# Performance work log

Hardware: AMD Instinct MI355X
Metric: run time of the kernel (lower is better)

Reference implementation:

```python
import jax, jax.numpy as jnp
import numpy as np

N = 100000   # nodes
E = 1600000  # edges
F = 256      # feature_dim
H = 64       # hidden_dim == out_channels
HEADS = 1


def setup_inputs() -> dict:
    key = jax.random.key(0)
    ks = jax.random.split(key, 12)
    x = jax.random.normal(ks[0], (N, F), dtype=jnp.float32)
    edge_index = jax.random.randint(ks[1], (2, E), 0, N, dtype=jnp.int32)
    s = 0.05
    params = {
        'W_proj': jax.random.normal(ks[2], (F, H), dtype=jnp.float32) * s,
        'b_proj': jnp.zeros((H,), dtype=jnp.float32),
        'Wq1': jax.random.normal(ks[3], (H, HEADS * H), dtype=jnp.float32) * s,
        'Wk1': jax.random.normal(ks[4], (H, HEADS * H), dtype=jnp.float32) * s,
        'Wv1': jax.random.normal(ks[5], (H, HEADS * H), dtype=jnp.float32) * s,
        'Wq2': jax.random.normal(ks[6], (H, HEADS * H), dtype=jnp.float32) * s,
        'Wk2': jax.random.normal(ks[7], (H, HEADS * H), dtype=jnp.float32) * s,
        'Wv2': jax.random.normal(ks[8], (H, HEADS * H), dtype=jnp.float32) * s,
        'W_sig': jax.random.normal(ks[9], (H, 1), dtype=jnp.float32) * s,
        'b_sig': jnp.zeros((1,), dtype=jnp.float32),
    }
    return {'x': x, 'edge_index': edge_index, **params}


def _gat_layer(x, src, dst, Wq, Wk, Wv):
    # x: [N, H]; src/dst: [E] (edge_index[0]=source j, edge_index[1]=dest i)
    n = x.shape[0]
    q = (x @ Wq).reshape(n, HEADS, H)
    k = (x @ Wk).reshape(n, HEADS, H)
    v = (x @ Wv).reshape(n, HEADS, H)
    # edge-wise scores: (q_i * k_j).sum(-1) / sqrt(out_channels)
    scores = jnp.einsum('ehc,ehc->eh', q[dst], k[src]) / np.float32(np.sqrt(H))
    alpha = jax.nn.relu(scores)                                  # [E, HEADS]
    # segment softmax over destination neighborhoods (numerically stable)
    m = jax.ops.segment_max(alpha, dst, num_segments=n)          # [N, HEADS]
    m = jnp.where(jnp.isfinite(m), m, jnp.float32(0.0))
    e = jnp.exp(alpha - m[dst])
    denom = jax.ops.segment_sum(e, dst, num_segments=n)
    a = e / (denom[dst] + jnp.float32(1e-16))                    # [E, HEADS]
    # scatter-weighted sum of values to destinations
    out = jax.ops.segment_sum(v[src] * a[:, :, None], dst, num_segments=n)
    return out.mean(axis=1), a                                   # [N, H], [E, HEADS]


def reference(x, edge_index, W_proj, b_proj, Wq1, Wk1, Wv1, Wq2, Wk2, Wv2, W_sig, b_sig):
    src, dst = edge_index[0], edge_index[1]
    h = jax.nn.gelu(x @ W_proj + b_proj, approximate=False)
    h, attn1 = _gat_layer(h, src, dst, Wq1, Wk1, Wv1)
    h = jax.nn.gelu(h, approximate=False)
    h, attn2 = _gat_layer(h, src, dst, Wq2, Wk2, Wv2)
    signals = h @ W_sig + b_sig                                  # [N, 1]
    return signals, attn1, attn2
```

## Files before the change

kernel.cpp:

```cpp
#include <hip/hip_runtime.h>
#include <hip/hip_fp16.h>
#include <math.h>

#define FF 256
#define HH 64

typedef __attribute__((ext_vector_type(8))) short short8;
typedef __attribute__((ext_vector_type(4))) float f32x4;

__device__ __forceinline__ float gelu_f(float x) {
    float ax = fabsf(x) * 0.70710678118654752f;
    float t = __builtin_amdgcn_rcpf(fmaf(0.3275911f, ax, 1.0f));
    float poly = t * fmaf(t, fmaf(t, fmaf(t, fmaf(t, 1.061405429f, -1.453152027f),
                  1.421413741f), -0.284496736f), 0.254829592f);
    float er = 1.0f - poly * __expf(-ax * ax);
    er = (x < 0.f) ? -er : er;
    return 0.5f * x * (1.0f + er);
}

__device__ __forceinline__ unsigned short bf16rne(float f) {
    unsigned u = __float_as_uint(f);
    unsigned r = u + 0x7FFFu + ((u >> 16) & 1u);
    return (unsigned short)(r >> 16);
}

__device__ __forceinline__ void bf16split(float f, short& hi, short& lo) {
    unsigned u = __float_as_uint(f);
    unsigned r = u + 0x7FFFu + ((u >> 16) & 1u);
    hi = (short)(r >> 16);
    float fh = __uint_as_float(r & 0xFFFF0000u);
    float fl = f - fh;
    unsigned u2 = __float_as_uint(fl);
    unsigned r2 = u2 + 0x7FFFu + ((u2 >> 16) & 1u);
    lo = (short)(r2 >> 16);
}

__device__ __forceinline__ __half2 shfl_xor_h2(__half2 v, int off) {
    union { __half2 h; int i; } u;
    u.h = v;
    u.i = __shfl_xor(u.i, off, 64);
    return u.h;
}

__global__ __launch_bounds__(256) void k_wprep(
        const float* __restrict__ Wp,
        const float* __restrict__ Wq1, const float* __restrict__ Wk1, const float* __restrict__ Wv1,
        const float* __restrict__ Wq2, const float* __restrict__ Wk2, const float* __restrict__ Wv2,
        short* __restrict__ wf) {
    int total = 16384 + 6 * 4096;
    for (int gid = blockIdx.x * 256 + threadIdx.x; gid < total; gid += gridDim.x * 256) {
        const float* W;
        int fid, hibase, lobase;
        if (gid < 16384) {
            W = Wp; fid = gid; hibase = 0; lobase = 16384;
        } else {
            int t = gid - 16384;
            int m = t >> 12;
            fid = t & 4095;
            switch (m) {
                case 0: W = Wq1; break;
                case 1: W = Wk1; break;
                case 2: W = Wv1; break;
                case 3: W = Wq2; break;
                case 4: W = Wk2; break;
                default: W = Wv2; break;
            }
            hibase = 32768 + m * 8192;
            lobase = hibase + 4096;
        }
        int j    = fid & 7;
        int lane = (fid >> 3) & 63;
        int ct   = (fid >> 9) & 3;
        int s    = fid >> 11;
        int k    = s * 32 + (lane >> 4) * 8 + j;
        int col  = ct * 16 + (lane & 15);
        short hi, lo;
        bf16split(W[k * HH + col], hi, lo);
        wf[hibase + fid] = hi;
        wf[lobase + fid] = lo;
    }
}

__device__ __forceinline__ void do_degree(int bid, const int* __restrict__ dst,
        int* __restrict__ deg, int* __restrict__ rank, int E) {
    int base = bid * 4096;
    if (base >= E) return;
    int e0 = base + threadIdx.x * 4;
    if (base + 4095 < E) {
        int4 d[4];
        #pragma unroll
        for (int i = 0; i < 4; ++i)
            d[i] = *reinterpret_cast<const int4*>(dst + e0 + i * 1024);
        int4 r[4];
        #pragma unroll
        for (int i = 0; i < 4; ++i) {
            r[i].x = atomicAdd(&deg[d[i].x], 1);
            r[i].y = atomicAdd(&deg[d[i].y], 1);
            r[i].z = atomicAdd(&deg[d[i].z], 1);
            r[i].w = atomicAdd(&deg[d[i].w], 1);
        }
        #pragma unroll
        for (int i = 0; i < 4; ++i)
            *reinterpret_cast<int4*>(rank + e0 + i * 1024) = r[i];
    } else {
        #pragma unroll
        for (int i = 0; i < 4; ++i)
            for (int j = 0; j < 4; ++j) {
                int e = e0 + i * 1024 + j;
                if (e < E) rank[e] = atomicAdd(&deg[dst[e]], 1);
            }
    }
}

__device__ __forceinline__ void do_fill(int bid, const int* __restrict__ src,
        const int* __restrict__ dst, const int* __restrict__ rowptr,
        const int* __restrict__ rank,
        int* __restrict__ esrc, int* __restrict__ inv, int E) {
    int base = bid * 4096;
    if (base >= E) return;
    int e0 = base + threadIdx.x * 4;
    if (base + 4095 < E) {
        int4 d[4], s[4], r[4];
        #pragma unroll
        for (int i = 0; i < 4; ++i) {
            d[i] = *reinterpret_cast<const int4*>(dst + e0 + i * 1024);
            s[i] = *reinterpret_cast<const int4*>(src + e0 + i * 1024);
            r[i] = *reinterpret_cast<const int4*>(rank + e0 + i * 1024);
        }
        int4 p[4];
        #pragma unroll
        for (int i = 0; i < 4; ++i) {
            p[i].x = rowptr[d[i].x] + r[i].x;
            p[i].y = rowptr[d[i].y] + r[i].y;
            p[i].z = rowptr[d[i].z] + r[i].z;
            p[i].w = rowptr[d[i].w] + r[i].w;
        }
        #pragma unroll
        for (int i = 0; i < 4; ++i) {
            esrc[p[i].x] = s[i].x;
            esrc[p[i].y] = s[i].y;
            esrc[p[i].z] = s[i].z;
            esrc[p[i].w] = s[i].w;
            *reinterpret_cast<int4*>(inv + e0 + i * 1024) = p[i];
        }
    } else {
        #pragma unroll
        for (int i = 0; i < 4; ++i)
            for (int j = 0; j < 4; ++j) {
                int e = e0 + i * 1024 + j;
                if (e < E) {
                    int pos = rowptr[dst[e]] + rank[e];
                    esrc[pos] = src[e];
                    inv[e] = pos;
                }
            }
    }
}

__device__ __forceinline__ void do_attn(int bid, const float* __restrict__ ecsr,
        const int* __restrict__ inv, float* __restrict__ attn, int E) {
    int e0 = (bid * 256 + threadIdx.x) * 4;
    if (e0 + 3 < E) {
        int4 i4 = *reinterpret_cast<const int4*>(inv + e0);
        float4 a;
        a.x = ecsr[i4.x]; a.y = ecsr[i4.y]; a.z = ecsr[i4.z]; a.w = ecsr[i4.w];
        *reinterpret_cast<float4*>(attn + e0) = a;
    } else {
        for (int e = e0; e < E; ++e) attn[e] = ecsr[inv[e]];
    }
}

__device__ __forceinline__ void do_proj(int bid, const float* __restrict__ x,
        const short* __restrict__ wf, const float* __restrict__ b,
        float* __restrict__ h, int n) {
    if (bid * 64 >= n) return;
    int lane = threadIdx.x & 63;
    int w    = threadIdx.x >> 6;
    int m    = lane & 15, g = lane >> 4;
    int rowc = min(bid * 64 + w * 16 + m, n - 1);
    const float* xrow = x + (size_t)rowc * FF + g * 8;
    const short* wlo = wf + 16384;
    f32x4 acc[4];
    #pragma unroll
    for (int ct = 0; ct < 4; ++ct) acc[ct] = (f32x4){0.f, 0.f, 0.f, 0.f};
    #pragma unroll
    for (int s = 0; s < 8; ++s) {
        float4 a0 = *reinterpret_cast<const float4*>(xrow + s * 32);
        float4 a1 = *reinterpret_cast<const float4*>(xrow + s * 32 + 4);
        float av[8] = {a0.x, a0.y, a0.z, a0.w, a1.x, a1.y, a1.z, a1.w};
        short8 ah, al;
        #pragma unroll
        for (int j = 0; j < 8; ++j) { short hi, lo; bf16split(av[j], hi, lo); ah[j] = hi; al[j] = lo; }
        #pragma unroll
        for (int ct = 0; ct < 4; ++ct) {
            int fo = ((s * 4 + ct) * 64 + lane) * 8;
            short8 bh = *reinterpret_cast<const short8*>(wf + fo);
            short8 bl = *reinterpret_cast<const short8*>(wlo + fo);
            acc[ct] = __builtin_amdgcn_mfma_f32_16x16x32_bf16(ah, bh, acc[ct], 0, 0, 0);
            acc[ct] = __builtin_amdgcn_mfma_f32_16x16x32_bf16(al, bh, acc[ct], 0, 0, 0);
            acc[ct] = __builtin_amdgcn_mfma_f32_16x16x32_bf16(ah, bl, acc[ct], 0, 0, 0);
        }
    }
    int orow0 = bid * 64 + w * 16 + g * 4;
    #pragma unroll
    for (int ct = 0; ct < 4; ++ct) {
        int col = ct * 16 + m;
        float bias = b[col];
        #pragma unroll
        for (int r = 0; r < 4; ++r) {
            int row = orow0 + r;
            if (row < n) h[(size_t)row * HH + col] = acc[ct][r] + bias;
        }
    }
}

__device__ __forceinline__ void do_qkv(int bid, const float* __restrict__ hsrc,
        const short* __restrict__ wfq, const short* __restrict__ wfk, const short* __restrict__ wfv,
        __half* __restrict__ qh, __half* __restrict__ kv, int n) {
    if (bid * 64 >= n) return;
    int lane = threadIdx.x & 63;
    int w    = threadIdx.x >> 6;
    int m    = lane & 15, g = lane >> 4;
    int rowc = min(bid * 64 + w * 16 + m, n - 1);
    const float* hrow = hsrc + (size_t)rowc * HH + g * 8;
    f32x4 aq[4], ak[4], av_[4];
    #pragma unroll
    for (int ct = 0; ct < 4; ++ct) {
        aq[ct] = (f32x4){0.f, 0.f, 0.f, 0.f};
        ak[ct] = (f32x4){0.f, 0.f, 0.f, 0.f};
        av_[ct] = (f32x4){0.f, 0.f, 0.f, 0.f};
    }
    #pragma unroll
    for (int s = 0; s < 2; ++s) {
        float4 a0 = *reinterpret_cast<const float4*>(hrow + s * 32);
        float4 a1 = *reinterpret_cast<const float4*>(hrow + s * 32 + 4);
        float avv[8] = {a0.x, a0.y, a0.z, a0.w, a1.x, a1.y, a1.z, a1.w};
        short8 ah;
        #pragma unroll
        for (int j = 0; j < 8; ++j) ah[j] = (short)bf16rne(gelu_f(avv[j]));
        #pragma unroll
        for (int ct = 0; ct < 4; ++ct) {
            int fo = ((s * 4 + ct) * 64 + lane) * 8;
            short8 qh8 = *reinterpret_cast<const short8*>(wfq + fo);
            short8 ql8 = *reinterpret_cast<const short8*>(wfq + 4096 + fo);
            short8 kh8 = *reinterpret_cast<const short8*>(wfk + fo);
            short8 kl8 = *reinterpret_cast<const short8*>(wfk + 4096 + fo);
            short8 vh8 = *reinterpret_cast<const short8*>(wfv + fo);
            short8 vl8 = *reinterpret_cast<const short8*>(wfv + 4096 + fo);
            aq[ct] = __builtin_amdgcn_mfma_f32_16x16x32_bf16(ah, qh8, aq[ct], 0, 0, 0);
            aq[ct] = __builtin_amdgcn_mfma_f32_16x16x32_bf16(ah, ql8, aq[ct], 0, 0, 0);
            ak[ct] = __builtin_amdgcn_mfma_f32_16x16x32_bf16(ah, kh8, ak[ct], 0, 0, 0);
            ak[ct] = __builtin_amdgcn_mfma_f32_16x16x32_bf16(ah, kl8, ak[ct], 0, 0, 0);
            av_[ct] = __builtin_amdgcn_mfma_f32_16x16x32_bf16(ah, vh8, av_[ct], 0, 0, 0);
            av_[ct] = __builtin_amdgcn_mfma_f32_16x16x32_bf16(ah, vl8, av_[ct], 0, 0, 0);
        }
    }
    int orow0 = bid * 64 + w * 16 + g * 4;
    #pragma unroll
    for (int ct = 0; ct < 4; ++ct) {
        int col = ct * 16 + m;
        int cb  = (col >> 3) * 16 + (col & 7);
        #pragma unroll
        for (int r = 0; r < 4; ++r) {
            int row = orow0 + r;
            if (row < n) {
                qh[(size_t)row * HH + col]     = __float2half(aq[ct][r]);
                kv[(size_t)row * 128 + cb]     = __float2half(ak[ct][r]);
                kv[(size_t)row * 128 + cb + 8] = __float2half(av_[ct][r]);
            }
        }
    }
}

__global__ __launch_bounds__(256) void k_proj_degree(
        const float* __restrict__ x, const short* __restrict__ wf,
        const float* __restrict__ b, float* __restrict__ h, int n,
        const int* __restrict__ dst, int* __restrict__ deg, int* __restrict__ rank, int E) {
    int bid = blockIdx.x >> 1;
    if ((blockIdx.x & 1) == 0) do_proj(bid, x, wf, b, h, n);
    else                       do_degree(bid, dst, deg, rank, E);
}

__global__ __launch_bounds__(256) void k_qkv_fill(
        const float* __restrict__ hsrc,
        const short* __restrict__ wfq, const short* __restrict__ wfk, const short* __restrict__ wfv,
        __half* __restrict__ qh, __half* __restrict__ kv, int n,
        const int* __restrict__ src, const int* __restrict__ dst,
        const int* __restrict__ rowptr, const int* __restrict__ rank,
        int* __restrict__ esrc, int* __restrict__ inv, int E) {
    int bid = blockIdx.x >> 1;
    if ((blockIdx.x & 1) == 0) do_qkv(bid, hsrc, wfq, wfk, wfv, qh, kv, n);
    else                       do_fill(bid, src, dst, rowptr, rank, esrc, inv, E);
}

__global__ __launch_bounds__(256) void k_qkv_attn(
        const float* __restrict__ hsrc,
        const short* __restrict__ wfq, const short* __restrict__ wfk, const short* __restrict__ wfv,
        __half* __restrict__ qh, __half* __restrict__ kv, int n,
        const float* __restrict__ ecsr, const int* __restrict__ inv,
        float* __restrict__ attn, int E) {
    int bid = blockIdx.x >> 1;
    if ((blockIdx.x & 1) == 0) do_qkv(bid, hsrc, wfq, wfk, wfv, qh, kv, n);
    else                       do_attn(bid, ecsr, inv, attn, E);
}

__global__ __launch_bounds__(256) void k_attn(const float* __restrict__ ecsr,
        const int* __restrict__ inv, float* __restrict__ attn, int E) {
    do_attn(blockIdx.x, ecsr, inv, attn, E);
}

__global__ __launch_bounds__(256) void k_scan1(const int* __restrict__ deg,
        int* __restrict__ out, int* __restrict__ bsums, int n) {
    __shared__ int lds[256];
    int t = threadIdx.x;
    int base = blockIdx.x * 1024 + t * 4;
    int v0 = (base     < n) ? deg[base]     : 0;
    int v1 = (base + 1 < n) ? deg[base + 1] : 0;
    int v2 = (base + 2 < n) ? deg[base + 2] : 0;
    int v3 = (base + 3 < n) ? deg[base + 3] : 0;
    int s = v0 + v1 + v2 + v3;
    int val = s;
    lds[t] = val;
    __syncthreads();
    #pragma unroll
    for (int off = 1; off < 256; off <<= 1) {
        int tmp = (t >= off) ? lds[t - off] : 0;
        __syncthreads();
        val += tmp;
        lds[t] = val;
        __syncthreads();
    }
    if (t == 255) bsums[blockIdx.x] = val;
    int excl = val - s;
    if (base     < n) out[base]     = excl;
    if (base + 1 < n) out[base + 1] = excl + v0;
    if (base + 2 < n) out[base + 2] = excl + v0 + v1;
    if (base + 3 < n) out[base + 3] = excl + v0 + v1 + v2;
}

__global__ __launch_bounds__(256) void k_scan2(const int* __restrict__ bsums,
        int* __restrict__ boffs, int nb) {
    __shared__ int lds[256];
    int t = threadIdx.x;
    int s = (t < nb) ? bsums[t] : 0;
    int val = s;
    lds[t] = val;
    __syncthreads();
    #pragma unroll
    for (int off = 1; off < 256; off <<= 1) {
        int tmp = (t >= off) ? lds[t - off] : 0;
        __syncthreads();
        val += tmp;
        lds[t] = val;
        __syncthreads();
    }
    if (t < nb) boffs[t] = val - s;
}

__global__ __launch_bounds__(256) void k_scan3(int* __restrict__ rowptr,
        const int* __restrict__ boffs, int n, int E) {
    int i = blockIdx.x * 256 + threadIdx.x;
    if (i < n) rowptr[i] += boffs[i >> 10];
    if (i == n) rowptr[n] = E;
}

template<bool LAST>
__global__ __launch_bounds__(256) void k_edge(
        const __half* __restrict__ qarr, const __half* __restrict__ kv,
        const int* __restrict__ rowptr,
        const int* __restrict__ esrc,
        float* __restrict__ ecsr,
        float* __restrict__ hout,
        float* __restrict__ signals,
        const float* __restrict__ Wsig, const float* __restrict__ bsig,
        int n) {
    int node = blockIdx.x * 4 + (threadIdx.x >> 6);
    if (node >= n) return;
    int lane = threadIdx.x & 63;
    int li = lane & 7, g = lane >> 3;
    int start = rowptr[node], end = rowptr[node + 1];
    int deg = end - start;
    __half2 q2[4];
    {
        union { uint4 u; __half2 h[4]; } Q;
        Q.u = *reinterpret_cast<const uint4*>(qarr + (size_t)node * HH + li * 8);
        #pragma unroll
        for (int j = 0; j < 4; ++j) q2[j] = Q.h[j];
    }
    int p0 = start + lane;
    int el = (p0 < end) ? esrc[p0] : 0;

    __half2 acc2[4];
    #pragma unroll
    for (int j = 0; j < 4; ++j) acc2[j] = __float2half2_rn(0.f);
    float s = 0.f;
    for (int c = 0; c < deg; c += 16) {
        int idx0 = c + g, idx1 = c + 8 + g;
        bool v0 = idx0 < deg, v1 = idx1 < deg;
        int sv0, sv1;
        if (c + 16 <= 64) {
            sv0 = __shfl(el, idx0);
            sv1 = __shfl(el, idx1);
        } else {
            sv0 = v0 ? esrc[start + idx0] : 0;
            sv1 = v1 ? esrc[start + idx1] : 0;
        }
        const __half* b0 = kv + (size_t)sv0 * 128 + li * 16;
        const __half* b1 = kv + (size_t)sv1 * 128 + li * 16;
        union { uint4 u; __half2 h[4]; } K0, V0, K1, V1;
        K0.u = *reinterpret_cast<const uint4*>(b0);
        V0.u = *reinterpret_cast<const uint4*>(b0 + 8);
        K1.u = *reinterpret_cast<const uint4*>(b1);
        V1.u = *reinterpret_cast<const uint4*>(b1 + 8);
        __half2 d20 = __float2half2_rn(0.f);
        __half2 d21 = __float2half2_rn(0.f);
        #pragma unroll
        for (int j = 0; j < 4; ++j) {
            d20 = __hfma2(q2[j], K0.h[j], d20);
            d21 = __hfma2(q2[j], K1.h[j], d21);
        }
        float d0 = __low2float(d20) + __high2float(d20);
        float d1 = __low2float(d21) + __high2float(d21);
        d0 += __shfl_xor(d0, 1); d1 += __shfl_xor(d1, 1);
        d0 += __shfl_xor(d0, 2); d1 += __shfl_xor(d1, 2);
        d0 += __shfl_xor(d0, 4); d1 += __shfl_xor(d1, 4);
        float e0 = v0 ? __expf(fmaxf(d0 * 0.125f, 0.f)) : 0.f;
        float e1 = v1 ? __expf(fmaxf(d1 * 0.125f, 0.f)) : 0.f;
        s += e0 + e1;
        if (v0 && li == 0) ecsr[start + idx0] = e0;
        if (v1 && li == 0) ecsr[start + idx1] = e1;
        __half2 e20 = __float2half2_rn(e0);
        __half2 e21 = __float2half2_rn(e1);
        #pragma unroll
        for (int j = 0; j < 4; ++j) {
            acc2[j] = __hfma2(e20, V0.h[j], acc2[j]);
            acc2[j] = __hfma2(e21, V1.h[j], acc2[j]);
        }
    }
    #pragma unroll
    for (int off = 8; off < 64; off <<= 1) {
        s += __shfl_xor(s, off);
        #pragma unroll
        for (int j = 0; j < 4; ++j)
            acc2[j] = __hadd2(acc2[j], shfl_xor_h2(acc2[j], off));
    }
    float inv = 1.0f / (s + 1e-16f);
    float af[8];
    #pragma unroll
    for (int j = 0; j < 4; ++j) {
        af[2 * j]     = __low2float(acc2[j]);
        af[2 * j + 1] = __high2float(acc2[j]);
    }

    if (!LAST) {
        if (g == 0) {
            float4 o0, o1;
            o0.x = af[0] * inv; o0.y = af[1] * inv; o0.z = af[2] * inv; o0.w = af[3] * inv;
            o1.x = af[4] * inv; o1.y = af[5] * inv; o1.z = af[6] * inv; o1.w = af[7] * inv;
            *reinterpret_cast<float4*>(hout + (size_t)node * HH + li * 8)     = o0;
            *reinterpret_cast<float4*>(hout + (size_t)node * HH + li * 8 + 4) = o1;
        }
    } else {
        float4 w0 = *reinterpret_cast<const float4*>(Wsig + li * 8);
        float4 w1 = *reinterpret_cast<const float4*>(Wsig + li * 8 + 4);
        float t = af[0] * w0.x + af[1] * w0.y + af[2] * w0.z + af[3] * w0.w
                + af[4] * w1.x + af[5] * w1.y + af[6] * w1.z + af[7] * w1.w;
        t *= inv;
        t += __shfl_xor(t, 1);
        t += __shfl_xor(t, 2);
        t += __shfl_xor(t, 4);
        if (lane == 0) signals[node] = t + bsig[0];
    }
    for (int p = p0; p < end; p += 64)
        ecsr[p] *= inv;
}

extern "C" void kernel_launch(void* const* d_in, const int* in_sizes, int n_in,
                              void* d_out, int out_size, void* d_ws, size_t ws_size,
                              hipStream_t stream) {
    const float* x   = (const float*)d_in[0];
    const int*   ei  = (const int*)  d_in[1];
    const float* Wp  = (const float*)d_in[2];
    const float* bp  = (const float*)d_in[3];
    const float* Wq1 = (const float*)d_in[4];
    const float* Wk1 = (const float*)d_in[5];
    const float* Wv1 = (const float*)d_in[6];
    const float* Wq2 = (const float*)d_in[7];
    const float* Wk2 = (const float*)d_in[8];
    const float* Wv2 = (const float*)d_in[9];
    const float* Wsg = (const float*)d_in[10];
    const float* bsg = (const float*)d_in[11];

    const int N = in_sizes[0] / FF;
    const int E = in_sizes[1] / 2;
    const int* src = ei;
    const int* dst = ei + E;

    char* ws = (char*)d_ws;
    size_t off = 0;
    auto alloc = [&](size_t bytes) -> void* {
        void* p = ws + off;
        off += (bytes + 255) & ~(size_t)255;
        return p;
    };
    __half* qh   = (__half*)alloc((size_t)N * HH * 2);
    __half* kv   = (__half*)alloc((size_t)N * 128 * 2);
    float* h     = (float*)alloc((size_t)N * HH * 4);
    float* ecsr  = (float*)alloc((size_t)E * 4);
    int* inv     = (int*)alloc((size_t)E * 4);
    int* esrc    = (int*)alloc((size_t)E * 4);
    int* rank    = (int*)alloc((size_t)E * 4);
    int* deg     = (int*)alloc((size_t)N * 4);
    int* rowptr  = (int*)alloc((size_t)(N + 1) * 4);
    int* bsums   = (int*)alloc(256 * 4);
    int* boffs   = (int*)alloc(256 * 4);
    short* wf    = (short*)alloc((size_t)81920 * 2);

    float* out     = (float*)d_out;
    float* signals = out;
    float* attn1   = out + N;
    float* attn2   = out + N + E;

    k_wprep<<<64, 256, 0, stream>>>(Wp, Wq1, Wk1, Wv1, Wq2, Wk2, Wv2, wf);
    hipMemsetAsync(deg, 0, (size_t)N * 4, stream);

    int gemmBlocks = (N + 63) / 64;
    int e4Blocks   = ((E + 3) / 4 + 255) / 256;
    int fusedGrid  = 2 * gemmBlocks;

    k_proj_degree<<<fusedGrid, 256, 0, stream>>>(x, wf, bp, h, N, dst, deg, rank, E);

    int nb = (N + 1023) / 1024;
    k_scan1<<<nb, 256, 0, stream>>>(deg, rowptr, bsums, N);
    k_scan2<<<1, 256, 0, stream>>>(bsums, boffs, nb);
    k_scan3<<<(N + 1 + 255) / 256, 256, 0, stream>>>(rowptr, boffs, N, E);

    const short* wfbase = wf + 32768;
    k_qkv_fill<<<fusedGrid, 256, 0, stream>>>(h, wfbase, wfbase + 8192, wfbase + 16384,
            qh, kv, N, src, dst, rowptr, rank, esrc, inv, E);
    k_edge<false><<<(N + 3) / 4, 256, 0, stream>>>(qh, kv, rowptr, esrc,
            ecsr, h, nullptr, nullptr, nullptr, N);

    k_qkv_attn<<<fusedGrid, 256, 0, stream>>>(h, wfbase + 24576, wfbase + 32768, wfbase + 40960,
            qh, kv, N, ecsr, inv, attn1, E);
    k_edge<true><<<(N + 3) / 4, 256, 0, stream>>>(qh, kv, rowptr, esrc,
            ecsr, nullptr, signals, Wsg, bsg, N);
    k_attn<<<e4Blocks, 256, 0, stream>>>(ecsr, inv, attn2, E);
}
```

Baseline: 311.5 us.

## Build CSR via two-level bucket partition instead of global atomic degree counting

```diff
diff --git a/kernel.cpp b/kernel.cpp
--- a/kernel.cpp
+++ b/kernel.cpp
@@ -81,79 +81,199 @@
     }
 }
 
-__device__ __forceinline__ void do_degree(int bid, const int* __restrict__ dst,
-        int* __restrict__ deg, int* __restrict__ rank, int E) {
+
+__global__ __launch_bounds__(256) void k_partA(const int* __restrict__ dst,
+        int* __restrict__ blockHist, int E, int PB, int NB) {
+    __shared__ int hist[256];
+    int t = threadIdx.x, bid = blockIdx.x;
+    hist[t] = 0;
+    __syncthreads();
     int base = bid * 4096;
-    if (base >= E) return;
-    int e0 = base + threadIdx.x * 4;
+    int e0 = base + t * 4;
     if (base + 4095 < E) {
-        int4 d[4];
-        #pragma unroll
-        for (int i = 0; i < 4; ++i)
-            d[i] = *reinterpret_cast<const int4*>(dst + e0 + i * 1024);
-        int4 r[4];
         #pragma unroll
         for (int i = 0; i < 4; ++i) {
-            r[i].x = atomicAdd(&deg[d[i].x], 1);
-            r[i].y = atomicAdd(&deg[d[i].y], 1);
-            r[i].z = atomicAdd(&deg[d[i].z], 1);
-            r[i].w = atomicAdd(&deg[d[i].w], 1);
-        }
-        #pragma unroll
-        for (int i = 0; i < 4; ++i)
-            *reinterpret_cast<int4*>(rank + e0 + i * 1024) = r[i];
+            int4 d = *reinterpret_cast<const int4*>(dst + e0 + i * 1024);
+            atomicAdd(&hist[d.x >> 9], 1);
+            atomicAdd(&hist[d.y >> 9], 1);
+            atomicAdd(&hist[d.z >> 9], 1);
+            atomicAdd(&hist[d.w >> 9], 1);
+        }
     } else {
-        #pragma unroll
         for (int i = 0; i < 4; ++i)
             for (int j = 0; j < 4; ++j) {
                 int e = e0 + i * 1024 + j;
-                if (e < E) rank[e] = atomicAdd(&deg[dst[e]], 1);
+                if (e < E) atomicAdd(&hist[dst[e] >> 9], 1);
             }
     }
-}
-
-__device__ __forceinline__ void do_fill(int bid, const int* __restrict__ src,
-        const int* __restrict__ dst, const int* __restrict__ rowptr,
-        const int* __restrict__ rank,
-        int* __restrict__ esrc, int* __restrict__ inv, int E) {
+    __syncthreads();
+    if (t < NB) blockHist[t * PB + bid] = hist[t];
+}
+
+__global__ __launch_bounds__(512) void k_partA2(int* __restrict__ blockHist,
+        int* __restrict__ bucketTotal, int PB) {
+    __shared__ int buf[512];
+    int t = threadIdx.x, b = blockIdx.x;
+    int orig = (t < PB) ? blockHist[b * PB + t] : 0;
+    buf[t] = orig;
+    __syncthreads();
+    #pragma unroll
+    for (int off = 1; off < 512; off <<= 1) {
+        int v = (t >= off) ? buf[t - off] : 0;
+        __syncthreads();
+        buf[t] += v;
+        __syncthreads();
+    }
+    if (t < PB) blockHist[b * PB + t] = buf[t] - orig;
+    if (t == 511) bucketTotal[b] = buf[511];
+}
+
+__global__ __launch_bounds__(256) void k_partA2b(const int* __restrict__ bucketTotal,
+        int* __restrict__ bucketBase, int* __restrict__ rowptr, int NB, int N, int E) {
+    __shared__ int buf[256];
+    int t = threadIdx.x;
+    int orig = (t < NB) ? bucketTotal[t] : 0;
+    buf[t] = orig;
+    __syncthreads();
+    #pragma unroll
+    for (int off = 1; off < 256; off <<= 1) {
+        int v = (t >= off) ? buf[t - off] : 0;
+        __syncthreads();
+        buf[t] += v;
+        __syncthreads();
+    }
+    if (t < NB) bucketBase[t] = buf[t] - orig;
+    if (t == 0) { bucketBase[NB] = buf[255]; rowptr[N] = E; }
+}
+
+__device__ __forceinline__ void do_partB(int bid, const int* __restrict__ src,
+        const int* __restrict__ dst, const int* __restrict__ blockBase,
+        const int* __restrict__ bucketBase,
+        int* __restrict__ bps, int* __restrict__ beid, int E, int PB, int NB) {
+    if (bid >= PB) return;
+    __shared__ int hist[256], lstart[256], cur[256], basec[256];
+    __shared__ int spack[4096], seid_[4096], gtar[4096];
+    int t = threadIdx.x;
+    hist[t] = 0;
+    __syncthreads();
     int base = bid * 4096;
-    if (base >= E) return;
-    int e0 = base + threadIdx.x * 4;
-    if (base + 4095 < E) {
-        int4 d[4], s[4], r[4];
+    int e0 = base + t * 4;
+    bool full = (base + 4095 < E);
+    if (full) {
         #pragma unroll
         for (int i = 0; i < 4; ++i) {
-            d[i] = *reinterpret_cast<const int4*>(dst + e0 + i * 1024);
-            s[i] = *reinterpret_cast<const int4*>(src + e0 + i * 1024);
-            r[i] = *reinterpret_cast<const int4*>(rank + e0 + i * 1024);
-        }
-        int4 p[4];
-        #pragma unroll
-        for (int i = 0; i < 4; ++i) {
-            p[i].x = rowptr[d[i].x] + r[i].x;
-            p[i].y = rowptr[d[i].y] + r[i].y;
-            p[i].z = rowptr[d[i].z] + r[i].z;
-            p[i].w = rowptr[d[i].w] + r[i].w;
-        }
-        #pragma unroll
-        for (int i = 0; i < 4; ++i) {
-            esrc[p[i].x] = s[i].x;
-            esrc[p[i].y] = s[i].y;
-            esrc[p[i].z] = s[i].z;
-            esrc[p[i].w] = s[i].w;
-            *reinterpret_cast<int4*>(inv + e0 + i * 1024) = p[i];
+            int4 d = *reinterpret_cast<const int4*>(dst + e0 + i * 1024);
+            atomicAdd(&hist[d.x >> 9], 1);
+            atomicAdd(&hist[d.y >> 9], 1);
+            atomicAdd(&hist[d.z >> 9], 1);
+            atomicAdd(&hist[d.w >> 9], 1);
         }
     } else {
-        #pragma unroll
         for (int i = 0; i < 4; ++i)
             for (int j = 0; j < 4; ++j) {
                 int e = e0 + i * 1024 + j;
-                if (e < E) {
-                    int pos = rowptr[dst[e]] + rank[e];
-                    esrc[pos] = src[e];
-                    inv[e] = pos;
-                }
+                if (e < E) atomicAdd(&hist[dst[e] >> 9], 1);
             }
+    }
+    __syncthreads();
+    int h0 = hist[t];
+    lstart[t] = h0;
+    __syncthreads();
+    #pragma unroll
+    for (int off = 1; off < 256; off <<= 1) {
+        int v = (t >= off) ? lstart[t - off] : 0;
+        __syncthreads();
+        lstart[t] += v;
+        __syncthreads();
+    }
+    int excl = lstart[t] - h0;
+    __syncthreads();
+    lstart[t] = excl;
+    cur[t]    = excl;
+    basec[t]  = (t < NB) ? (bucketBase[t] + blockBase[t * PB + bid] - excl) : 0;
+    __syncthreads();
+    auto place = [&](int d, int s, int e) {
+        int bu = d >> 9;
+        int pos = atomicAdd(&cur[bu], 1);
+        spack[pos] = ((d & 511) << 17) | s;
+        seid_[pos] = e;
+        gtar[pos]  = basec[bu] + pos;
+    };
+    if (full) {
+        #pragma unroll
+        for (int i = 0; i < 4; ++i) {
+            int4 d = *reinterpret_cast<const int4*>(dst + e0 + i * 1024);
+            int4 s = *reinterpret_cast<const int4*>(src + e0 + i * 1024);
+            int eb = e0 + i * 1024;
+            place(d.x, s.x, eb);
+            place(d.y, s.y, eb + 1);
+            place(d.z, s.z, eb + 2);
+            place(d.w, s.w, eb + 3);
+        }
+    } else {
+        for (int i = 0; i < 4; ++i)
+            for (int j = 0; j < 4; ++j) {
+                int e = e0 + i * 1024 + j;
+                if (e < E) place(dst[e], src[e], e);
+            }
+    }
+    __syncthreads();
+    int count = min(4096, E - base);
+    #pragma unroll
+    for (int i = 0; i < 16; ++i) {
+        int sidx = t + i * 256;
+        if (sidx < count) {
+            int g = gtar[sidx];
+            bps[g]  = spack[sidx];
+            beid[g] = seid_[sidx];
+        }
+    }
+}
+
+__device__ __forceinline__ void do_partC(int b, const int* __restrict__ bps,
+        const int* __restrict__ beid, const int* __restrict__ bucketBase,
+        int* __restrict__ rowptr, int* __restrict__ esrc, int* __restrict__ inv,
+        int N, int NB) {
+    if (b >= NB) return;
+    __shared__ int cnt[512], sc[512], cur[512], pairbuf[256];
+    int t = threadIdx.x;
+    cnt[t] = 0; cnt[t + 256] = 0;
+    cur[t] = 0; cur[t + 256] = 0;
+    __syncthreads();
+    int rB = bucketBase[b], rE = bucketBase[b + 1];
+    for (int p = rB + t; p < rE; p += 256)
+        atomicAdd(&cnt[bps[p] >> 17], 1);
+    __syncthreads();
+    int a  = cnt[2 * t], b2 = cnt[2 * t + 1];
+    int ps = a + b2;
+    pairbuf[t] = ps;
+    __syncthreads();
+    #pragma unroll
+    for (int off = 1; off < 256; off <<= 1) {
+        int v = (t >= off) ? pairbuf[t - off] : 0;
+        __syncthreads();
+        pairbuf[t] += v;
+        __syncthreads();
+    }
+    int pex = pairbuf[t] - ps;
+    sc[2 * t]     = pex;
+    sc[2 * t + 1] = pex + a;
+    __syncthreads();
+    int lo = b << 9;
+    #pragma unroll
+    for (int i = 0; i < 2; ++i) {
+        int idx = t + i * 256;
+        int node = lo + idx;
+        if (node < N) rowptr[node] = rB + sc[idx];
+    }
+    for (int p = rB + t; p < rE; p += 256) {
+        int u = bps[p];
+        int local = u >> 17;
+        int s = u & 0x1FFFF;
+        int r = atomicAdd(&cur[local], 1);
+        int pos = rB + sc[local] + r;
+        esrc[pos] = s;
+        inv[beid[p]] = pos;
     }
 }
 
@@ -272,25 +392,27 @@
     }
 }
 
-__global__ __launch_bounds__(256) void k_proj_degree(
+__global__ __launch_bounds__(256) void k_proj_partB(
         const float* __restrict__ x, const short* __restrict__ wf,
         const float* __restrict__ b, float* __restrict__ h, int n,
-        const int* __restrict__ dst, int* __restrict__ deg, int* __restrict__ rank, int E) {
+        const int* __restrict__ src, const int* __restrict__ dst,
+        const int* __restrict__ blockBase, const int* __restrict__ bucketBase,
+        int* __restrict__ bps, int* __restrict__ beid, int E, int PB, int NB) {
     int bid = blockIdx.x >> 1;
     if ((blockIdx.x & 1) == 0) do_proj(bid, x, wf, b, h, n);
-    else                       do_degree(bid, dst, deg, rank, E);
-}
-
-__global__ __launch_bounds__(256) void k_qkv_fill(
+    else                       do_partB(bid, src, dst, blockBase, bucketBase, bps, beid, E, PB, NB);
+}
+
+__global__ __launch_bounds__(256) void k_qkv_partC(
         const float* __restrict__ hsrc,
         const short* __restrict__ wfq, const short* __restrict__ wfk, const short* __restrict__ wfv,
         __half* __restrict__ qh, __half* __restrict__ kv, int n,
-        const int* __restrict__ src, const int* __restrict__ dst,
-        const int* __restrict__ rowptr, const int* __restrict__ rank,
-        int* __restrict__ esrc, int* __restrict__ inv, int E) {
+        const int* __restrict__ bps, const int* __restrict__ beid,
+        const int* __restrict__ bucketBase,
+        int* __restrict__ rowptr, int* __restrict__ esrc, int* __restrict__ inv, int NB) {
     int bid = blockIdx.x >> 1;
     if ((blockIdx.x & 1) == 0) do_qkv(bid, hsrc, wfq, wfk, wfv, qh, kv, n);
-    else                       do_fill(bid, src, dst, rowptr, rank, esrc, inv, E);
+    else                       do_partC(bid, bps, beid, bucketBase, rowptr, esrc, inv, n, NB);
 }
 
 __global__ __launch_bounds__(256) void k_qkv_attn(
@@ -307,61 +429,6 @@
 __global__ __launch_bounds__(256) void k_attn(const float* __restrict__ ecsr,
         const int* __restrict__ inv, float* __restrict__ attn, int E) {
     do_attn(blockIdx.x, ecsr, inv, attn, E);
-}
-
-__global__ __launch_bounds__(256) void k_scan1(const int* __restrict__ deg,
-        int* __restrict__ out, int* __restrict__ bsums, int n) {
-    __shared__ int lds[256];
-    int t = threadIdx.x;
-    int base = blockIdx.x * 1024 + t * 4;
-    int v0 = (base     < n) ? deg[base]     : 0;
-    int v1 = (base + 1 < n) ? deg[base + 1] : 0;
-    int v2 = (base + 2 < n) ? deg[base + 2] : 0;
-    int v3 = (base + 3 < n) ? deg[base + 3] : 0;
-    int s = v0 + v1 + v2 + v3;
-    int val = s;
-    lds[t] = val;
-    __syncthreads();
-    #pragma unroll
-    for (int off = 1; off < 256; off <<= 1) {
-        int tmp = (t >= off) ? lds[t - off] : 0;
-        __syncthreads();
-        val += tmp;
-        lds[t] = val;
-        __syncthreads();
-    }
-    if (t == 255) bsums[blockIdx.x] = val;
-    int excl = val - s;
-    if (base     < n) out[base]     = excl;
-    if (base + 1 < n) out[base + 1] = excl + v0;
-    if (base + 2 < n) out[base + 2] = excl + v0 + v1;
-    if (base + 3 < n) out[base + 3] = excl + v0 + v1 + v2;
-}
-
-__global__ __launch_bounds__(256) void k_scan2(const int* __restrict__ bsums,
-        int* __restrict__ boffs, int nb) {
-    __shared__ int lds[256];
-    int t = threadIdx.x;
-    int s = (t < nb) ? bsums[t] : 0;
-    int val = s;
-    lds[t] = val;
-    __syncthreads();
-    #pragma unroll
-    for (int off = 1; off < 256; off <<= 1) {
-        int tmp = (t >= off) ? lds[t - off] : 0;
-        __syncthreads();
-        val += tmp;
-        lds[t] = val;
-        __syncthreads();
-    }
-    if (t < nb) boffs[t] = val - s;
-}
-
-__global__ __launch_bounds__(256) void k_scan3(int* __restrict__ rowptr,
-        const int* __restrict__ boffs, int n, int E) {
-    int i = blockIdx.x * 256 + threadIdx.x;
-    if (i < n) rowptr[i] += boffs[i >> 10];
-    if (i == n) rowptr[n] = E;
 }
 
 template<bool LAST>
@@ -496,6 +563,9 @@
     const int* src = ei;
     const int* dst = ei + E;
 
+    const int NB = (N + 511) >> 9;
+    const int PB = (E + 4095) >> 12;
+
     char* ws = (char*)d_ws;
     size_t off = 0;
     auto alloc = [&](size_t bytes) -> void* {
@@ -509,11 +579,12 @@
     float* ecsr  = (float*)alloc((size_t)E * 4);
     int* inv     = (int*)alloc((size_t)E * 4);
     int* esrc    = (int*)alloc((size_t)E * 4);
-    int* rank    = (int*)alloc((size_t)E * 4);
-    int* deg     = (int*)alloc((size_t)N * 4);
+    int* bps     = (int*)alloc((size_t)E * 4);
+    int* beid    = (int*)alloc((size_t)E * 4);
     int* rowptr  = (int*)alloc((size_t)(N + 1) * 4);
-    int* bsums   = (int*)alloc(256 * 4);
-    int* boffs   = (int*)alloc(256 * 4);
+    int* blockHist   = (int*)alloc((size_t)NB * PB * 4);
+    int* bucketTotal = (int*)alloc((size_t)NB * 4);
+    int* bucketBase  = (int*)alloc((size_t)(NB + 1) * 4);
     short* wf    = (short*)alloc((size_t)81920 * 2);
 
     float* out     = (float*)d_out;
@@ -522,26 +593,27 @@
     float* attn2   = out + N + E;
 
     k_wprep<<<64, 256, 0, stream>>>(Wp, Wq1, Wk1, Wv1, Wq2, Wk2, Wv2, wf);
-    hipMemsetAsync(deg, 0, (size_t)N * 4, stream);
+
+    k_partA<<<PB, 256, 0, stream>>>(dst, blockHist, E, PB, NB);
+    k_partA2<<<NB, 512, 0, stream>>>(blockHist, bucketTotal, PB);
+    k_partA2b<<<1, 256, 0, stream>>>(bucketTotal, bucketBase, rowptr, NB, N, E);
 
     int gemmBlocks = (N + 63) / 64;
     int e4Blocks   = ((E + 3) / 4 + 255) / 256;
-    int fusedGrid  = 2 * gemmBlocks;
-
-    k_proj_degree<<<fusedGrid, 256, 0, stream>>>(x, wf, bp, h, N, dst, deg, rank, E);
-
-    int nb = (N + 1023) / 1024;
-    k_scan1<<<nb, 256, 0, stream>>>(deg, rowptr, bsums, N);
-    k_scan2<<<1, 256, 0, stream>>>(bsums, boffs, nb);
-    k_scan3<<<(N + 1 + 255) / 256, 256, 0, stream>>>(rowptr, boffs, N, E);
+    int fusedB     = 2 * max(gemmBlocks, PB);
+    int fusedC     = 2 * max(gemmBlocks, NB);
+    int fusedA     = 2 * max(gemmBlocks, e4Blocks);
+
+    k_proj_partB<<<fusedB, 256, 0, stream>>>(x, wf, bp, h, N,
+            src, dst, blockHist, bucketBase, bps, beid, E, PB, NB);
 
     const short* wfbase = wf + 32768;
-    k_qkv_fill<<<fusedGrid, 256, 0, stream>>>(h, wfbase, wfbase + 8192, wfbase + 16384,
-            qh, kv, N, src, dst, rowptr, rank, esrc, inv, E);
+    k_qkv_partC<<<fusedC, 256, 0, stream>>>(h, wfbase, wfbase + 8192, wfbase + 16384,
+            qh, kv, N, bps, beid, bucketBase, rowptr, esrc, inv, NB);
     k_edge<false><<<(N + 3) / 4, 256, 0, stream>>>(qh, kv, rowptr, esrc,
             ecsr, h, nullptr, nullptr, nullptr, N);
 
-    k_qkv_attn<<<fusedGrid, 256, 0, stream>>>(h, wfbase + 24576, wfbase + 32768, wfbase + 40960,
+    k_qkv_attn<<<fusedA, 256, 0, stream>>>(h, wfbase + 24576, wfbase + 32768, wfbase + 40960,
             qh, kv, N, ecsr, inv, attn1, E);
     k_edge<true><<<(N + 3) / 4, 256, 0, stream>>>(qh, kv, rowptr, esrc,
             ecsr, nullptr, signals, Wsg, bsg, N);
```

After: 313.8 us. Within noise of the previous version (+0.7%).
